# Optimization experiments

Measured on AMD Instinct MI355X. Metric: run time of the kernel, lower is better.

Reference implementation:

```python
import jax, jax.numpy as jnp
import numpy as np

GROUPS = 32
EPS = 1e-6  # flax.linen.GroupNorm default


def group_norm(x, scale, bias):
    B, H, W, C = x.shape
    xg = x.reshape(B, H, W, GROUPS, C // GROUPS)
    mean = jnp.mean(xg, axis=(1, 2, 4), keepdims=True)
    var = jnp.var(xg, axis=(1, 2, 4), keepdims=True)
    xn = (xg - mean) * jax.lax.rsqrt(var + EPS)
    return xn.reshape(B, H, W, C) * scale + bias


def setup_inputs() -> dict:
    key = jax.random.key(0)
    ks = jax.random.split(key, 8)
    B, H, W, C = 8, 64, 64, 128
    s = C ** -0.5  # fan-in style init scale for 1x1 conv kernels
    return {
        "x": jax.random.normal(ks[0], (B, H, W, C), dtype=jnp.float32),
        "gn_scale": jnp.ones((C,), dtype=jnp.float32),
        "gn_bias": jnp.zeros((C,), dtype=jnp.float32),
        "wq": jax.random.normal(ks[1], (C, C), dtype=jnp.float32) * s,
        "bq": jnp.zeros((C,), dtype=jnp.float32),
        "wk": jax.random.normal(ks[2], (C, C), dtype=jnp.float32) * s,
        "bk": jnp.zeros((C,), dtype=jnp.float32),
        "wv": jax.random.normal(ks[3], (C, C), dtype=jnp.float32) * s,
        "bv": jnp.zeros((C,), dtype=jnp.float32),
        "wo": jax.random.normal(ks[4], (C, C), dtype=jnp.float32) * s,
        "bo": jnp.zeros((C,), dtype=jnp.float32),
    }


def reference(x, gn_scale, gn_bias, wq, bq, wk, bk, wv, bv, wo, bo):
    B, H, W, C = x.shape
    N = H * W
    h = group_norm(x, gn_scale, gn_bias)                       # [B,H,W,C]
    hf = h.reshape(B, N, C)
    q = hf @ wq + bq                                           # 1x1 conv == per-position matmul
    k = hf @ wk + bk
    v = hf @ wv + bv
    w_ = jnp.einsum('bqd,bkd->bqk', q, k) * (C ** -0.5)        # [B,N,N] full score matrix
    w_ = jax.nn.softmax(w_, axis=2)
    o = jnp.einsum('bqk,bkd->bqd', w_, v)                      # [B,N,C]
    o = o @ wo + bo
    return x + o.reshape(B, H, W, C)
```

## Files before the change

kernel.cpp:

```cpp
#include <hip/hip_runtime.h>
#include <hip/hip_bf16.h>

#define NN 4096
#define CC 128
#define SCALE 0.088388347648318447f
#define LOG2E 1.4426950408889634f

typedef __attribute__((ext_vector_type(8))) short short8v;
typedef __attribute__((ext_vector_type(4))) float f32x4;
typedef __attribute__((ext_vector_type(16))) float f32x16;

#define Z16 {0.f,0.f,0.f,0.f,0.f,0.f,0.f,0.f,0.f,0.f,0.f,0.f,0.f,0.f,0.f,0.f}

__device__ __forceinline__ short f2bf(float f) {
  unsigned u = __float_as_uint(f);
  u = (u + 0x7FFFu + ((u >> 16) & 1u)) >> 16;
  return (short)u;
}
__device__ __forceinline__ float bf2f(short s) {
  return __uint_as_float(((unsigned)(unsigned short)s) << 16);
}
__device__ __forceinline__ unsigned pk2bf(float lo, float hi) {
  unsigned r;
  asm("v_cvt_pk_bf16_f32 %0, %1, %2" : "=v"(r) : "v"(lo), "v"(hi));
  return r;
}
__device__ __forceinline__ f32x4 mfma16(short8v a, short8v b, f32x4 c) {
  return __builtin_amdgcn_mfma_f32_16x16x32_bf16(a, b, c, 0, 0, 0);
}
__device__ __forceinline__ f32x16 mfma32(short8v a, short8v b, f32x16 c) {
  return __builtin_amdgcn_mfma_f32_32x32x16_bf16(a, b, c, 0, 0, 0);
}
__device__ __forceinline__ void gload16(const void* g, void* l) {
  __builtin_amdgcn_global_load_lds(
      (const __attribute__((address_space(1))) unsigned*)g,
      (__attribute__((address_space(3))) unsigned*)l, 16, 0, 0);
}

__global__ __launch_bounds__(256) void prep_k(
    const float* __restrict__ x,
    const float* __restrict__ wq, const float* __restrict__ wk,
    const float* __restrict__ wv, const float* __restrict__ wo,
    const float* __restrict__ bq, short* __restrict__ wT,
    float* __restrict__ bqs, float* __restrict__ macc,
    float* __restrict__ vacc) {
  if (blockIdx.x >= 256) {
    int gid = (blockIdx.x - 256) * 256 + threadIdx.x;
    int widx = gid >> 14, e = gid & 16383;
    int kk = e >> 7, n = e & 127;
    const float* src = (widx == 0) ? wq : (widx == 1) ? wk
                     : (widx == 2) ? wv : wo;
    float v = src[kk * 128 + n];
    if (widx == 0) v *= SCALE * LOG2E;
    wT[widx * 16384 + n * 128 + kk] = f2bf(v);
    if (gid < 128) bqs[gid] = bq[gid] * SCALE * LOG2E;
    return;
  }
  int b = blockIdx.x >> 5, rc = blockIdx.x & 31;
  const float4* xp = reinterpret_cast<const float4*>(
      x + (size_t)b * NN * CC + (size_t)rc * 128 * CC);
  int tid = threadIdx.x;
  float s = 0.f, ss = 0.f;
  #pragma unroll
  for (int j = 0; j < 16; ++j) {
    float4 v = xp[tid + 256 * j];
    s  += v.x + v.y + v.z + v.w;
    ss += v.x * v.x + v.y * v.y + v.z * v.z + v.w * v.w;
  }
  __shared__ float as_[256], ass_[256];
  as_[tid] = s; ass_[tid] = ss;
  __syncthreads();
  if (tid < 32) {
    float ts = 0.f, tss = 0.f;
    #pragma unroll
    for (int j = 0; j < 8; ++j) { ts += as_[tid + 32 * j]; tss += ass_[tid + 32 * j]; }
    atomicAdd(&macc[b * 32 + tid], ts);
    atomicAdd(&vacc[b * 32 + tid], tss);
  }
}

__global__ __launch_bounds__(256) void fqkv_k(
    const float* __restrict__ x, const float* __restrict__ macc,
    const float* __restrict__ vacc, const float* __restrict__ gsc,
    const float* __restrict__ gbi, const short* __restrict__ wT,
    const float* __restrict__ bqs, const float* __restrict__ bk,
    const float* __restrict__ bv, short* __restrict__ qout,
    short* __restrict__ kout, short* __restrict__ vtout) {
  __shared__ short wlds[128][136];
  int lane = threadIdx.x & 63, wid = threadIdx.x >> 6;
  int row0 = blockIdx.x * 64 + wid * 16;
  int arow = row0 + (lane & 15);
  int q4 = lane >> 4;
  int bidx = arow >> 12;
  short8v a[4];
  #pragma unroll
  for (int dt = 0; dt < 4; ++dt) {
    int c0 = dt * 32 + q4 * 8;
    float4 v0 = *reinterpret_cast<const float4*>(x + (size_t)arow * CC + c0);
    float4 v1 = *reinterpret_cast<const float4*>(x + (size_t)arow * CC + c0 + 4);
    int g0 = bidx * 32 + (c0 >> 2);
    float mu0 = macc[g0] * (1.f / 16384.f);
    float r0 = rsqrtf(vacc[g0] * (1.f / 16384.f) - mu0 * mu0 + 1e-6f);
    float mu1 = macc[g0 + 1] * (1.f / 16384.f);
    float r1 = rsqrtf(vacc[g0 + 1] * (1.f / 16384.f) - mu1 * mu1 + 1e-6f);
    float4 s0 = *reinterpret_cast<const float4*>(gsc + c0);
    float4 s1 = *reinterpret_cast<const float4*>(gsc + c0 + 4);
    float4 b0 = *reinterpret_cast<const float4*>(gbi + c0);
    float4 b1 = *reinterpret_cast<const float4*>(gbi + c0 + 4);
    union { short s[8]; short8v v; } pk;
    pk.s[0] = f2bf((v0.x - mu0) * r0 * s0.x + b0.x);
    pk.s[1] = f2bf((v0.y - mu0) * r0 * s0.y + b0.y);
    pk.s[2] = f2bf((v0.z - mu0) * r0 * s0.z + b0.z);
    pk.s[3] = f2bf((v0.w - mu0) * r0 * s0.w + b0.w);
    pk.s[4] = f2bf((v1.x - mu1) * r1 * s1.x + b1.x);
    pk.s[5] = f2bf((v1.y - mu1) * r1 * s1.y + b1.y);
    pk.s[6] = f2bf((v1.z - mu1) * r1 * s1.z + b1.z);
    pk.s[7] = f2bf((v1.w - mu1) * r1 * s1.w + b1.w);
    a[dt] = pk.v;
  }
  for (int ph = 0; ph < 3; ++ph) {
    if (ph) __syncthreads();
    const short* w = wT + ph * 16384;
    for (int i = threadIdx.x; i < 2048; i += 256) {
      int n = i >> 4, kk = (i & 15) << 3;
      *reinterpret_cast<short8v*>(&wlds[n][kk]) =
          *reinterpret_cast<const short8v*>(w + n * 128 + kk);
    }
    __syncthreads();
    const float* bias = (ph == 0) ? bqs : (ph == 1) ? bk : bv;
    f32x4 zero = {0.f, 0.f, 0.f, 0.f};
    f32x4 acc[8];
    #pragma unroll
    for (int nt = 0; nt < 8; ++nt) acc[nt] = zero;
    #pragma unroll
    for (int nt = 0; nt < 8; ++nt) {
      #pragma unroll
      for (int kk = 0; kk < 4; ++kk) {
        short8v b = *reinterpret_cast<const short8v*>(
            &wlds[nt * 16 + (lane & 15)][kk * 32 + q4 * 8]);
        acc[nt] = mfma16(a[kk], b, acc[nt]);
      }
    }
    short* dst = (ph == 0) ? qout : (ph == 1) ? kout : vtout;
    #pragma unroll
    for (int nt = 0; nt < 8; ++nt) {
      #pragma unroll
      for (int r = 0; r < 4; ++r) {
        int row = row0 + q4 * 4 + r;
        int col = nt * 16 + (lane & 15);
        float v = acc[nt][r] + bias[col];
        if (ph == 2) {
          int b_ = row >> 12, n = row & 4095;
          dst[((size_t)b_ * 128 + col) * 4096 + n] = f2bf(v);
        } else {
          dst[(size_t)row * 128 + col] = f2bf(v);
        }
      }
    }
  }
}

template <int S>
__global__ __launch_bounds__(256, 3) void attn5_k(
    const short* __restrict__ q, const short* __restrict__ k,
    const short* __restrict__ vt, short* __restrict__ opart,
    float* __restrict__ ls) {
  constexpr int KVLEN = NN / S;
  constexpr int NIT = KVLEN / 32;
  __shared__ short8v smem_v[2048];
  char* smem = (char*)smem_v;
  const int tid = threadIdx.x;
  const int lane = tid & 63, warp = tid >> 6;
  const int hh = lane >> 5, ql = lane & 31;
  const int split = (int)blockIdx.x % S;
  const int qb_lin = (int)blockIdx.x / S;
  const int b = qb_lin >> 5, qblk = qb_lin & 31;
  const int kv0 = split * KVLEN;

  const size_t bqko = (size_t)b * NN * CC;
  short8v qf[8];
  {
    int qrow = qblk * 128 + warp * 32 + ql;
    const short* qp = q + bqko + (size_t)qrow * CC + hh * 8;
    #pragma unroll
    for (int dc = 0; dc < 8; ++dc)
      qf[dc] = *reinterpret_cast<const short8v*>(qp + dc * 16);
  }
  const char* kg = (const char*)(k + bqko);
  const char* vg = (const char*)(vt + (size_t)b * CC * NN);

  auto stage = [&](int buf, int it) {
    const int kvo = kv0 + it * 32;
    char* base = smem + buf * 16384;
    #pragma unroll
    for (int p = 0; p < 2; ++p) {
      int c = p * 256 + warp * 64 + lane;
      int krow = c >> 4, kj = c & 15;
      gload16(kg + (size_t)(kvo + krow) * 256 + 16 * (kj ^ (krow & 7)),
              base + p * 4096 + warp * 1024);
      int vd = c >> 2, vj = c & 3;
      gload16(vg + (size_t)vd * (NN * 2) + (size_t)kvo * 2 +
                  16 * (vj ^ ((vd >> 1) & 3)),
              base + 8192 + p * 4096 + warp * 1024);
    }
  };

  f32x16 oacc[4] = {Z16, Z16, Z16, Z16};
  float l_run = 0.f;

  stage(0, 0);
  asm volatile("s_waitcnt vmcnt(0)" ::: "memory");
  __builtin_amdgcn_s_barrier();

  const int swzK = (ql & 7) << 4;
  const int swzV = (ql & 6) << 3;
  for (int it = 0; it < NIT; ++it) {
    const int cur = it & 1;
    if (it + 1 < NIT) stage(cur ^ 1, it + 1);

    const char* kr_p = smem + cur * 16384 + ql * 256;
    f32x16 sT = Z16;
    #pragma unroll
    for (int dc = 0; dc < 8; ++dc) {
      short8v kf = *reinterpret_cast<const short8v*>(
          kr_p + ((32 * dc + 16 * hh) ^ swzK));
      sT = mfma32(kf, qf[dc], sT);
    }

    float rsum = 0.f;
    #pragma unroll
    for (int r = 0; r < 16; ++r) {
      float p = exp2f(sT[r]);
      sT[r] = p; rsum += p;
    }
    l_run += rsum;

    const char* vb_ = smem + cur * 16384 + 8192;
    #pragma unroll
    for (int st = 0; st < 2; ++st) {
      union { unsigned u[4]; short8v v; } pu;
      #pragma unroll
      for (int w = 0; w < 4; ++w)
        pu.u[w] = pk2bf(sT[8 * st + 2 * w], sT[8 * st + 2 * w + 1]);
      const int o1 = (32 * st + 8 * hh) ^ swzV;
      const int o2 = (32 * st + 8 * hh + 16) ^ swzV;
      #pragma unroll
      for (int dt = 0; dt < 4; ++dt) {
        const char* vr_p = vb_ + (32 * dt + ql) * 64;
        union { unsigned long long d[2]; short8v v; } vf;
        vf.d[0] = *reinterpret_cast<const unsigned long long*>(vr_p + o1);
        vf.d[1] = *reinterpret_cast<const unsigned long long*>(vr_p + o2);
        oacc[dt] = mfma32(pu.v, vf.v, oacc[dt]);
      }
    }

    asm volatile("s_waitcnt vmcnt(0)" ::: "memory");
    __builtin_amdgcn_s_barrier();
  }

  l_run += __shfl_xor(l_run, 32);
  float rinv = 1.f / l_run;
  short* op = opart + ((size_t)(split * 8 + b) * NN + qblk * 128 + warp * 32) * CC;
  #pragma unroll
  for (int r = 0; r < 16; ++r) {
    int qp = (r & 3) + 8 * (r >> 2) + 4 * hh;
    float ri = __shfl(rinv, qp);
    #pragma unroll
    for (int dt = 0; dt < 4; ++dt)
      op[(size_t)qp * CC + 32 * dt + ql] = f2bf(oacc[dt][r] * ri);
  }
  if (hh == 0) {
    size_t ix = (size_t)(split * 8 + b) * NN + qblk * 128 + warp * 32 + ql;
    ls[ix] = l_run;
  }
}

template <int S>
__global__ __launch_bounds__(256) void projoc_k(const short* __restrict__ opart,
    const float* __restrict__ ls, const short* __restrict__ wT,
    const float* __restrict__ bias, const float* __restrict__ x,
    float* __restrict__ out) {
  __shared__ short wlds[128][136];
  int lane = threadIdx.x & 63, wid = threadIdx.x >> 6;
  for (int i = threadIdx.x; i < 2048; i += 256) {
    int n = i >> 4, kk = (i & 15) << 3;
    *reinterpret_cast<short8v*>(&wlds[n][kk]) =
        *reinterpret_cast<const short8v*>(wT + n * 128 + kk);
  }
  int row0 = blockIdx.x * 64 + wid * 16;
  int arow = row0 + (lane & 15);
  int q4 = lane >> 4;
  float wgt[S];
  {
    float tot = 0.f;
    #pragma unroll
    for (int s = 0; s < S; ++s) {
      wgt[s] = ls[(size_t)s * 32768 + arow];
      tot += wgt[s];
    }
    float inv = 1.f / tot;
    #pragma unroll
    for (int s = 0; s < S; ++s) wgt[s] *= inv;
  }
  short8v a[4];
  #pragma unroll
  for (int dt = 0; dt < 4; ++dt) {
    int c0 = dt * 32 + q4 * 8;
    float acc8[8] = {0.f, 0.f, 0.f, 0.f, 0.f, 0.f, 0.f, 0.f};
    #pragma unroll
    for (int s = 0; s < S; ++s) {
      short8v v = *reinterpret_cast<const short8v*>(
          opart + ((size_t)s * 32768 + arow) * CC + c0);
      #pragma unroll
      for (int e = 0; e < 8; ++e) acc8[e] += wgt[s] * bf2f(v[e]);
    }
    union { short s[8]; short8v v; } pk;
    #pragma unroll
    for (int e = 0; e < 8; ++e) pk.s[e] = f2bf(acc8[e]);
    a[dt] = pk.v;
  }
  __syncthreads();
  f32x4 zero = {0.f, 0.f, 0.f, 0.f};
  f32x4 acc[8];
  #pragma unroll
  for (int nt = 0; nt < 8; ++nt) acc[nt] = zero;
  #pragma unroll
  for (int nt = 0; nt < 8; ++nt) {
    #pragma unroll
    for (int kk = 0; kk < 4; ++kk) {
      short8v b = *reinterpret_cast<const short8v*>(
          &wlds[nt * 16 + (lane & 15)][kk * 32 + q4 * 8]);
      acc[nt] = mfma16(a[kk], b, acc[nt]);
    }
  }
  #pragma unroll
  for (int nt = 0; nt < 8; ++nt) {
    #pragma unroll
    for (int r = 0; r < 4; ++r) {
      int row = row0 + q4 * 4 + r;
      int col = nt * 16 + (lane & 15);
      out[(size_t)row * 128 + col] =
          acc[nt][r] + bias[col] + x[(size_t)row * 128 + col];
    }
  }
}

extern "C" void kernel_launch(void* const* d_in, const int* in_sizes, int n_in,
                              void* d_out, int out_size, void* d_ws, size_t ws_size,
                              hipStream_t stream) {
  (void)in_sizes; (void)n_in; (void)out_size;
  const float* x   = (const float*)d_in[0];
  const float* gsc = (const float*)d_in[1];
  const float* gbi = (const float*)d_in[2];
  const float* wq  = (const float*)d_in[3];
  const float* bq  = (const float*)d_in[4];
  const float* wk  = (const float*)d_in[5];
  const float* bk  = (const float*)d_in[6];
  const float* wv  = (const float*)d_in[7];
  const float* bv  = (const float*)d_in[8];
  const float* wo  = (const float*)d_in[9];
  const float* bo  = (const float*)d_in[10];
  float* out = (float*)d_out;

  char* ws = (char*)d_ws;
  constexpr size_t OFF_WT   = 0;
  constexpr size_t OFF_BQS  = 131072;
  constexpr size_t OFF_MACC = 131584;
  constexpr size_t OFF_VACC = 132608;
  constexpr size_t OFF_QB   = 133632;
  constexpr size_t OFF_KB   = OFF_QB + 8388608;
  constexpr size_t OFF_VT   = OFF_KB + 8388608;
  constexpr size_t OFF_OP   = OFF_VT + 8388608;
  constexpr size_t NEED2 = OFF_OP + 2 * 8388608 + 2 * 131072;

  short* wT   = (short*)(ws + OFF_WT);
  float* bqs  = (float*)(ws + OFF_BQS);
  float* macc = (float*)(ws + OFF_MACC);
  float* vacc = (float*)(ws + OFF_VACC);
  short* qb   = (short*)(ws + OFF_QB);
  short* kb   = (short*)(ws + OFF_KB);
  short* vtb  = (short*)(ws + OFF_VT);
  short* opart= (short*)(ws + OFF_OP);
  const int S = (ws_size >= NEED2) ? 2 : 1;
  float* ls = (float*)(ws + OFF_OP + (size_t)S * 8388608);

  hipMemsetAsync(ws + OFF_MACC, 0, 2048, stream);
  prep_k<<<512, 256, 0, stream>>>(x, wq, wk, wv, wo, bq, wT, bqs, macc, vacc);
  fqkv_k<<<512, 256, 0, stream>>>(x, macc, vacc, gsc, gbi, wT, bqs, bk, bv,
                                  qb, kb, vtb);
  if (S == 2) {
    attn5_k<2><<<512, 256, 0, stream>>>(qb, kb, vtb, opart, ls);
    projoc_k<2><<<512, 256, 0, stream>>>(opart, ls, wT + 49152, bo, x, out);
  } else {
    attn5_k<1><<<256, 256, 0, stream>>>(qb, kb, vtb, opart, ls);
    projoc_k<1><<<512, 256, 0, stream>>>(opart, ls, wT + 49152, bo, x, out);
  }
}
```

Before: 126.8 us.

## Process two KV tiles per barrier with double-buffered tile pairs in attention

```diff
diff --git a/kernel.cpp b/kernel.cpp
--- a/kernel.cpp
+++ b/kernel.cpp
@@ -161,13 +161,13 @@
 }
 
 template <int S>
-__global__ __launch_bounds__(256, 3) void attn5_k(
+__global__ __launch_bounds__(256, 2) void attn10_k(
     const short* __restrict__ q, const short* __restrict__ k,
     const short* __restrict__ vt, short* __restrict__ opart,
     float* __restrict__ ls) {
   constexpr int KVLEN = NN / S;
   constexpr int NIT = KVLEN / 32;
-  __shared__ short8v smem_v[2048];
+  __shared__ short8v smem_v[4096];
   char* smem = (char*)smem_v;
   const int tid = threadIdx.x;
   const int lane = tid & 63, warp = tid >> 6;
@@ -207,18 +207,11 @@
 
   f32x16 oacc[4] = {Z16, Z16, Z16, Z16};
   float l_run = 0.f;
-
-  stage(0, 0);
-  asm volatile("s_waitcnt vmcnt(0)" ::: "memory");
-  __builtin_amdgcn_s_barrier();
-
   const int swzK = (ql & 7) << 4;
   const int swzV = (ql & 6) << 3;
-  for (int it = 0; it < NIT; ++it) {
-    const int cur = it & 1;
-    if (it + 1 < NIT) stage(cur ^ 1, it + 1);
-
-    const char* kr_p = smem + cur * 16384 + ql * 256;
+
+  auto tile = [&](const char* tb) {
+    const char* kr_p = tb + ql * 256;
     f32x16 sT = Z16;
     #pragma unroll
     for (int dc = 0; dc < 8; ++dc) {
@@ -226,7 +219,6 @@
           kr_p + ((32 * dc + 16 * hh) ^ swzK));
       sT = mfma32(kf, qf[dc], sT);
     }
-
     float rsum = 0.f;
     #pragma unroll
     for (int r = 0; r < 16; ++r) {
@@ -234,8 +226,7 @@
       sT[r] = p; rsum += p;
     }
     l_run += rsum;
-
-    const char* vb_ = smem + cur * 16384 + 8192;
+    const char* vb_ = tb + 8192;
     #pragma unroll
     for (int st = 0; st < 2; ++st) {
       union { unsigned u[4]; short8v v; } pu;
@@ -253,9 +244,21 @@
         oacc[dt] = mfma32(pu.v, vf.v, oacc[dt]);
       }
     }
-
-    asm volatile("s_waitcnt vmcnt(0)" ::: "memory");
-    __builtin_amdgcn_s_barrier();
+  };
+
+  stage(0, 0);
+  stage(1, 1);
+  __syncthreads();
+
+  for (int it = 0; it < NIT; it += 2) {
+    const int pc = (it >> 1) & 1;
+    if (it + 2 < NIT) {
+      stage((pc ^ 1) * 2, it + 2);
+      stage((pc ^ 1) * 2 + 1, it + 3);
+    }
+    tile(smem + (pc * 2) * 16384);
+    tile(smem + (pc * 2 + 1) * 16384);
+    __syncthreads();
   }
 
   l_run += __shfl_xor(l_run, 32);
@@ -389,10 +392,10 @@
   fqkv_k<<<512, 256, 0, stream>>>(x, macc, vacc, gsc, gbi, wT, bqs, bk, bv,
                                   qb, kb, vtb);
   if (S == 2) {
-    attn5_k<2><<<512, 256, 0, stream>>>(qb, kb, vtb, opart, ls);
+    attn10_k<2><<<512, 256, 0, stream>>>(qb, kb, vtb, opart, ls);
     projoc_k<2><<<512, 256, 0, stream>>>(opart, ls, wT + 49152, bo, x, out);
   } else {
-    attn5_k<1><<<256, 256, 0, stream>>>(qb, kb, vtb, opart, ls);
+    attn10_k<1><<<256, 256, 0, stream>>>(qb, kb, vtb, opart, ls);
     projoc_k<1><<<512, 256, 0, stream>>>(opart, ls, wT + 49152, bo, x, out);
   }
 }
```

Result: slower. 130.3 us (+2.7%).

## Split attention output dims across warp pairs, halving query rows per block

Applied to the files above, without the earlier changes.

```diff
diff --git a/kernel.cpp b/kernel.cpp
--- a/kernel.cpp
+++ b/kernel.cpp
@@ -161,7 +161,7 @@
 }
 
 template <int S>
-__global__ __launch_bounds__(256, 3) void attn5_k(
+__global__ __launch_bounds__(256, 4) void attn11_k(
     const short* __restrict__ q, const short* __restrict__ k,
     const short* __restrict__ vt, short* __restrict__ opart,
     float* __restrict__ ls) {
@@ -172,15 +172,16 @@
   const int tid = threadIdx.x;
   const int lane = tid & 63, warp = tid >> 6;
   const int hh = lane >> 5, ql = lane & 31;
+  const int qgrp = warp >> 1, dhalf = warp & 1;
   const int split = (int)blockIdx.x % S;
   const int qb_lin = (int)blockIdx.x / S;
-  const int b = qb_lin >> 5, qblk = qb_lin & 31;
+  const int b = qb_lin >> 6, qblk = qb_lin & 63;
   const int kv0 = split * KVLEN;
 
   const size_t bqko = (size_t)b * NN * CC;
   short8v qf[8];
   {
-    int qrow = qblk * 128 + warp * 32 + ql;
+    int qrow = qblk * 64 + qgrp * 32 + ql;
     const short* qp = q + bqko + (size_t)qrow * CC + hh * 8;
     #pragma unroll
     for (int dc = 0; dc < 8; ++dc)
@@ -205,7 +206,7 @@
     }
   };
 
-  f32x16 oacc[4] = {Z16, Z16, Z16, Z16};
+  f32x16 oacc[2] = {Z16, Z16};
   float l_run = 0.f;
 
   stage(0, 0);
@@ -245,12 +246,12 @@
       const int o1 = (32 * st + 8 * hh) ^ swzV;
       const int o2 = (32 * st + 8 * hh + 16) ^ swzV;
       #pragma unroll
-      for (int dt = 0; dt < 4; ++dt) {
-        const char* vr_p = vb_ + (32 * dt + ql) * 64;
+      for (int dtl = 0; dtl < 2; ++dtl) {
+        const char* vr_p = vb_ + (32 * (2 * dhalf + dtl) + ql) * 64;
         union { unsigned long long d[2]; short8v v; } vf;
         vf.d[0] = *reinterpret_cast<const unsigned long long*>(vr_p + o1);
         vf.d[1] = *reinterpret_cast<const unsigned long long*>(vr_p + o2);
-        oacc[dt] = mfma32(pu.v, vf.v, oacc[dt]);
+        oacc[dtl] = mfma32(pu.v, vf.v, oacc[dtl]);
       }
     }
 
@@ -260,18 +261,19 @@
 
   l_run += __shfl_xor(l_run, 32);
   float rinv = 1.f / l_run;
-  short* op = opart + ((size_t)(split * 8 + b) * NN + qblk * 128 + warp * 32) * CC;
+  size_t row0 = (size_t)(split * 8 + b) * NN + qblk * 64 + qgrp * 32;
+  short* op = opart + row0 * CC;
   #pragma unroll
   for (int r = 0; r < 16; ++r) {
     int qp = (r & 3) + 8 * (r >> 2) + 4 * hh;
     float ri = __shfl(rinv, qp);
     #pragma unroll
-    for (int dt = 0; dt < 4; ++dt)
-      op[(size_t)qp * CC + 32 * dt + ql] = f2bf(oacc[dt][r] * ri);
-  }
-  if (hh == 0) {
-    size_t ix = (size_t)(split * 8 + b) * NN + qblk * 128 + warp * 32 + ql;
-    ls[ix] = l_run;
+    for (int dtl = 0; dtl < 2; ++dtl)
+      op[(size_t)qp * CC + 32 * (2 * dhalf + dtl) + ql] =
+          f2bf(oacc[dtl][r] * ri);
+  }
+  if (dhalf == 0 && hh == 0) {
+    ls[row0 + ql] = l_run;
   }
 }
 
@@ -389,10 +391,10 @@
   fqkv_k<<<512, 256, 0, stream>>>(x, macc, vacc, gsc, gbi, wT, bqs, bk, bv,
                                   qb, kb, vtb);
   if (S == 2) {
-    attn5_k<2><<<512, 256, 0, stream>>>(qb, kb, vtb, opart, ls);
+    attn11_k<2><<<1024, 256, 0, stream>>>(qb, kb, vtb, opart, ls);
     projoc_k<2><<<512, 256, 0, stream>>>(opart, ls, wT + 49152, bo, x, out);
   } else {
-    attn5_k<1><<<256, 256, 0, stream>>>(qb, kb, vtb, opart, ls);
+    attn11_k<1><<<512, 256, 0, stream>>>(qb, kb, vtb, opart, ls);
     projoc_k<1><<<512, 256, 0, stream>>>(opart, ls, wT + 49152, bo, x, out);
   }
 }
```

Result: slower. 177.5 us (+40.0%).
